# Optimization experiments

Hardware: AMD Instinct MI355X
Metric: run time of the kernel (lower is better)

The kernel has to match this reference:

```python
import jax, jax.numpy as jnp
import numpy as np

DIM = 256
HEADS = 8
HEAD_DIM = DIM // HEADS
B_, N = 8192, 49


def setup_inputs() -> dict:
    key = jax.random.key(0)
    k1, k2, k3, k4, k5, k6 = jax.random.split(key, 6)
    x = jax.random.normal(k1, (B_, N, DIM), dtype=jnp.float32)
    mask = jax.random.normal(k2, (B_, N, N), dtype=jnp.float32)
    s = 1.0 / np.sqrt(DIM)
    W_qkv = jax.random.normal(k3, (3 * DIM, DIM), dtype=jnp.float32) * s
    b_qkv = jax.random.normal(k4, (3 * DIM,), dtype=jnp.float32) * 0.02
    W_proj = jax.random.normal(k5, (DIM, DIM), dtype=jnp.float32) * s
    b_proj = jax.random.normal(k6, (DIM,), dtype=jnp.float32) * 0.02
    return {"x": x, "mask": mask, "W_qkv": W_qkv, "b_qkv": b_qkv,
            "W_proj": W_proj, "b_proj": b_proj}


def reference(x, mask, W_qkv, b_qkv, W_proj, b_proj):
    B, n, C = x.shape
    scale = HEAD_DIM ** (-0.5)
    # qkv projection: (B, N, 3C) -> (3, B, H, N, hd)
    qkv = x @ W_qkv.T + b_qkv
    qkv = qkv.reshape(B, n, 3, HEADS, HEAD_DIM).transpose(2, 0, 3, 1, 4)
    q, k, v = qkv[0], qkv[1], qkv[2]
    # scaled dot-product within each window
    attn = jnp.einsum('bhqd,bhkd->bhqk', q, k) * scale
    attn = attn + mask[:, None, :, :]  # additive window mask
    attn = jax.nn.softmax(attn, axis=-1)
    out = jnp.einsum('bhqk,bhkd->bhqd', attn, v)
    out = out.transpose(0, 2, 1, 3).reshape(B, n, C)
    return out @ W_proj.T + b_proj
```

## Files before the change

kernel.cpp:

```cpp
#include <hip/hip_runtime.h>
#include <hip/hip_bf16.h>

#define NTOK 49
#define DIMC 256

typedef __attribute__((ext_vector_type(8))) short bf16x8;
typedef __attribute__((ext_vector_type(4))) float f32x4;

static __device__ __forceinline__ unsigned pk2(float a, float b) {
    union { __hip_bfloat16 h; unsigned short u; } ua, ub;
    ua.h = __float2bfloat16(a);
    ub.h = __float2bfloat16(b);
    return (unsigned)ua.u | ((unsigned)ub.u << 16);
}

static __device__ __forceinline__ bf16x8 mkfrag(unsigned w0, unsigned w1, unsigned w2, unsigned w3) {
    union { bf16x8 v; unsigned u[4]; } t;
    t.u[0] = w0; t.u[1] = w1; t.u[2] = w2; t.u[3] = w3;
    return t.v;
}

static __device__ __forceinline__ unsigned sel2(unsigned lo, unsigned hi, int src, int ghi) {
    unsigned a = __shfl(lo, src);
    unsigned b = __shfl(hi, src);
    return ghi ? b : a;
}

__global__ void convert_weights(const float* __restrict__ wq, const float* __restrict__ wp,
                                unsigned short* __restrict__ wqb, unsigned short* __restrict__ wpb) {
    int i = blockIdx.x * 256 + threadIdx.x;
    if (i < 768 * 256) {
        union { __hip_bfloat16 h; unsigned short u; } t;
        t.h = __float2bfloat16(wq[i]);
        wqb[i] = t.u;
    }
    if (i < 256 * 256) {
        union { __hip_bfloat16 h; unsigned short u; } t;
        t.h = __float2bfloat16(wp[i]);
        wpb[i] = t.u;
    }
}

__launch_bounds__(1024, 4)
__attribute__((amdgpu_waves_per_eu(4, 4)))
__global__ void win_attn_fused(const float* __restrict__ x, const float* __restrict__ mask,
                               const unsigned short* __restrict__ wqkv, const float* __restrict__ bqkv,
                               const unsigned short* __restrict__ wproj, const float* __restrict__ bproj,
                               float* __restrict__ out) {
    __shared__ __align__(16) char lds[131072];
    char* const xb  = lds;
    char* const kqv = lds + 32768;

    const int b = blockIdx.x;
    const int tid = threadIdx.x;
    const int lane = tid & 63;
    const int wid = tid >> 6;
    const int c = lane & 15;
    const int g = lane >> 4;
    const int h = wid >> 1;
    const int qh = wid & 1;
    const int srcA = c + 16 * ((2 * g) & 3);
    const int srcB = c + 16 * ((2 * g + 1) & 3);
    const int ghi = g >> 1;
    const float scale = 0.17677669529663687f;
    const f32x4 fzero = {0.f, 0.f, 0.f, 0.f};

    {
        const float* xw = x + (size_t)b * (NTOK * DIMC);
        #pragma unroll
        for (int it = 0; it < 4; ++it) {
            int idx = it * 1024 + tid;
            int t = idx >> 6;
            int d0 = (idx & 63) * 4;
            float4 v = make_float4(0.f, 0.f, 0.f, 0.f);
            if (t < NTOK) v = *(const float4*)(xw + t * DIMC + d0);
            *(uint2*)(xb + t * 512 + ((d0 * 2) ^ ((t & 7) << 4))) =
                make_uint2(pk2(v.x, v.y), pk2(v.z, v.w));
        }
    }
    __syncthreads();

    #define XFR(base_, t_, kk_) \
        (*(const bf16x8*)((base_) + (t_) * 512 + ((2 * ((kk_) + 8 * g)) ^ (((t_) & 7) << 4))))

    char* const Kh = kqv + h * 12288;
    char* const Qh = Kh + 4096;
    char* const Vh = Kh + 8192;

    {
        f32x4 aKQ[2][4], aV[4];
        #pragma unroll
        for (int md = 0; md < 2; ++md)
            #pragma unroll
            for (int j2 = 0; j2 < 4; ++j2) aKQ[md][j2] = fzero;
        #pragma unroll
        for (int mt = 0; mt < 4; ++mt) aV[mt] = fzero;

        const int woff = qh ? (h * 32) : (256 + h * 32);
        const unsigned short* wkq_base = wqkv + (size_t)(woff + c) * 256 + 8 * g;
        const unsigned short* wv_base  = wqkv + (size_t)(512 + h * 32 + qh * 16 + c) * 256 + 8 * g;
        #pragma unroll
        for (int ks = 0; ks < 8; ++ks) {
            int kk = ks * 32;
            bf16x8 xf[4];
            #pragma unroll
            for (int tt = 0; tt < 4; ++tt) { int t = tt * 16 + c; xf[tt] = XFR(xb, t, kk); }
            bf16x8 wkq0 = *(const bf16x8*)(wkq_base + kk);
            bf16x8 wkq1 = *(const bf16x8*)(wkq_base + 16 * 256 + kk);
            bf16x8 wv   = *(const bf16x8*)(wv_base + kk);
            #pragma unroll
            for (int j2 = 0; j2 < 4; ++j2) {
                aKQ[0][j2] = __builtin_amdgcn_mfma_f32_16x16x32_bf16(wkq0, xf[j2], aKQ[0][j2], 0, 0, 0);
                aKQ[1][j2] = __builtin_amdgcn_mfma_f32_16x16x32_bf16(wkq1, xf[j2], aKQ[1][j2], 0, 0, 0);
                aV[j2]     = __builtin_amdgcn_mfma_f32_16x16x32_bf16(xf[j2], wv, aV[j2], 0, 0, 0);
            }
        }

        char* kqdst = Kh + qh * 4096;
        const float* bb = bqkv + (qh ? 0 : 256) + h * 32;
        #pragma unroll
        for (int md = 0; md < 2; ++md) {
            const float* b4 = bb + md * 16 + 4 * g;
            float b0 = b4[0], b1 = b4[1], b2 = b4[2], b3 = b4[3];
            #pragma unroll
            for (int j2 = 0; j2 < 4; ++j2) {
                int t = j2 * 16 + c;
                int d0 = md * 16 + 4 * g;
                f32x4 v = aKQ[md][j2];
                float v0 = v[0] + b0, v1 = v[1] + b1, v2 = v[2] + b2, v3 = v[3] + b3;
                if (qh) { v0 *= scale; v1 *= scale; v2 *= scale; v3 *= scale; }
                *(uint2*)(kqdst + t * 64 + ((d0 * 2) ^ ((t & 3) << 4))) =
                    make_uint2(pk2(v0, v1), pk2(v2, v3));
            }
        }
        float bv = bqkv[512 + h * 32 + qh * 16 + c];
        #pragma unroll
        for (int mt = 0; mt < 4; ++mt) {
            int t0 = mt * 16 + 4 * g;
            int d = qh * 16 + c;
            f32x4 v = aV[mt];
            *(uint2*)(Vh + d * 128 + ((t0 * 2) ^ ((d & 7) << 4))) =
                make_uint2(pk2(v[0] + bv, v[1] + bv), pk2(v[2] + bv, v[3] + bv));
        }
    }
    __syncthreads();

    f32x4 oacc[2][2];
    {
        const float* mw = mask + (size_t)b * (NTOK * NTOK);
        f32x4 mv[2][3];
        float m48[2];
        #pragma unroll
        for (int jl = 0; jl < 2; ++jl) {
            int q = (qh * 2 + jl) * 16 + c;
            int qc = (q < NTOK) ? q : (NTOK - 1);
            const float* mrow = mw + qc * NTOK;
            mv[jl][0] = *(const f32x4*)(mrow + 0 + g * 4);
            mv[jl][1] = *(const f32x4*)(mrow + 16 + g * 4);
            mv[jl][2] = *(const f32x4*)(mrow + 32 + g * 4);
            m48[jl] = mrow[48];
        }

        bf16x8 ka[4], qf[2], vf[2][2];
        #pragma unroll
        for (int it = 0; it < 4; ++it) {
            int key = it * 16 + c;
            ka[it] = *(const bf16x8*)(Kh + key * 64 + ((g * 16) ^ ((key & 3) << 4)));
        }
        #pragma unroll
        for (int jl = 0; jl < 2; ++jl) {
            int q = (qh * 2 + jl) * 16 + c;
            qf[jl] = *(const bf16x8*)(Qh + q * 64 + ((g * 16) ^ ((q & 3) << 4)));
        }
        #pragma unroll
        for (int kh = 0; kh < 2; ++kh)
            #pragma unroll
            for (int dt = 0; dt < 2; ++dt) {
                int d = dt * 16 + c;
                vf[kh][dt] = *(const bf16x8*)(Vh + d * 128 +
                                              (((kh * 32 + g * 8) * 2) ^ ((d & 7) << 4)));
            }
        #pragma unroll
        for (int dt = 0; dt < 2; ++dt)
            #pragma unroll
            for (int jl = 0; jl < 2; ++jl) oacc[dt][jl] = fzero;

        #pragma unroll
        for (int jl = 0; jl < 2; ++jl) {
            float p[4][4];
            {
                f32x4 s = __builtin_amdgcn_mfma_f32_16x16x32_bf16(ka[0], qf[jl], fzero, 0, 0, 0);
                #pragma unroll
                for (int r = 0; r < 4; ++r) p[0][r] = s[r] + mv[jl][0][r];
            }
            {
                f32x4 s = __builtin_amdgcn_mfma_f32_16x16x32_bf16(ka[1], qf[jl], fzero, 0, 0, 0);
                #pragma unroll
                for (int r = 0; r < 4; ++r) p[1][r] = s[r] + mv[jl][1][r];
            }
            {
                f32x4 s = __builtin_amdgcn_mfma_f32_16x16x32_bf16(ka[2], qf[jl], fzero, 0, 0, 0);
                #pragma unroll
                for (int r = 0; r < 4; ++r) p[2][r] = s[r] + mv[jl][2][r];
            }
            {
                f32x4 s = __builtin_amdgcn_mfma_f32_16x16x32_bf16(ka[3], qf[jl], fzero, 0, 0, 0);
                #pragma unroll
                for (int r = 0; r < 4; ++r)
                    p[3][r] = (g == 0 && r == 0) ? (s[0] + m48[jl]) : -1e30f;
            }
            float m = -1e30f;
            #pragma unroll
            for (int it = 0; it < 4; ++it)
                #pragma unroll
                for (int r = 0; r < 4; ++r) m = fmaxf(m, p[it][r]);
            m = fmaxf(m, __shfl_xor(m, 16));
            m = fmaxf(m, __shfl_xor(m, 32));
            float ssum = 0.f;
            #pragma unroll
            for (int it = 0; it < 4; ++it)
                #pragma unroll
                for (int r = 0; r < 4; ++r) {
                    float e = __expf(p[it][r] - m);
                    p[it][r] = e;
                    ssum += e;
                }
            ssum += __shfl_xor(ssum, 16);
            ssum += __shfl_xor(ssum, 32);
            float inv = 1.0f / ssum;
            unsigned pq[4][2];
            #pragma unroll
            for (int it = 0; it < 4; ++it) {
                pq[it][0] = pk2(p[it][0] * inv, p[it][1] * inv);
                pq[it][1] = pk2(p[it][2] * inv, p[it][3] * inv);
            }
            #pragma unroll
            for (int kh = 0; kh < 2; ++kh) {
                bf16x8 pf = mkfrag(sel2(pq[2 * kh][0], pq[2 * kh + 1][0], srcA, ghi),
                                   sel2(pq[2 * kh][1], pq[2 * kh + 1][1], srcA, ghi),
                                   sel2(pq[2 * kh][0], pq[2 * kh + 1][0], srcB, ghi),
                                   sel2(pq[2 * kh][1], pq[2 * kh + 1][1], srcB, ghi));
                #pragma unroll
                for (int dt = 0; dt < 2; ++dt)
                    oacc[dt][jl] = __builtin_amdgcn_mfma_f32_16x16x32_bf16(vf[kh][dt], pf, oacc[dt][jl], 0, 0, 0);
            }
        }
    }

    #pragma unroll
    for (int dt = 0; dt < 2; ++dt) {
        #pragma unroll
        for (int jl = 0; jl < 2; ++jl) {
            int q = (qh * 2 + jl) * 16 + c;
            int d0 = h * 32 + dt * 16 + 4 * g;
            f32x4 v = oacc[dt][jl];
            *(uint2*)(xb + q * 512 + ((2 * d0) ^ ((q & 7) << 4))) =
                make_uint2(pk2(v[0], v[1]), pk2(v[2], v[3]));
        }
    }
    __syncthreads();

    {
        f32x4 pacc[4];
        #pragma unroll
        for (int mt = 0; mt < 4; ++mt) pacc[mt] = fzero;
        const int o = wid * 16 + c;
        const unsigned short* wp_base = wproj + (size_t)o * 256 + 8 * g;
        const float bias = bproj[o];
        #pragma unroll
        for (int ks = 0; ks < 8; ++ks) {
            int kk = ks * 32;
            bf16x8 bfr = *(const bf16x8*)(wp_base + kk);
            #pragma unroll
            for (int mt = 0; mt < 4; ++mt) {
                int t = mt * 16 + c;
                bf16x8 af = XFR(xb, t, kk);
                pacc[mt] = __builtin_amdgcn_mfma_f32_16x16x32_bf16(af, bfr, pacc[mt], 0, 0, 0);
            }
        }
        float* ob = out + (size_t)b * (NTOK * DIMC);
        #pragma unroll
        for (int mt = 0; mt < 4; ++mt) {
            #pragma unroll
            for (int r = 0; r < 4; ++r) {
                int t = mt * 16 + g * 4 + r;
                if (t < NTOK) ob[t * DIMC + o] = pacc[mt][r] + bias;
            }
        }
    }
    #undef XFR
}

extern "C" void kernel_launch(void* const* d_in, const int* in_sizes, int n_in,
                              void* d_out, int out_size, void* d_ws, size_t ws_size,
                              hipStream_t stream) {
    const float* x    = (const float*)d_in[0];
    const float* mask = (const float*)d_in[1];
    const float* wq   = (const float*)d_in[2];
    const float* bq   = (const float*)d_in[3];
    const float* wp   = (const float*)d_in[4];
    const float* bp   = (const float*)d_in[5];
    float* o = (float*)d_out;

    unsigned short* wqb = (unsigned short*)d_ws;
    unsigned short* wpb = wqb + 768 * 256;

    convert_weights<<<768, 256, 0, stream>>>(wq, wp, wqb, wpb);
    win_attn_fused<<<8192, 1024, 0, stream>>>(x, mask, wqb, bq, wpb, bp, o);
}
```

Measured before the change: 718.1 us.

## Halve block size to 512 threads, loop each wave over two heads

The fused window-attention kernel now runs 8 waves per block instead of 16. Each wave pair processes two heads in sequence, reusing a 48KB K/Q/V LDS region, so LDS drops from 128KB to 80KB per block. Attention outputs are kept in registers until both heads finish, and the output projection computes two column tiles per wave, reusing the A fragments. The goal is to fit more blocks per CU and reuse x fragments, at the cost of more per-block serialization, extra barriers and higher register pressure.

Result: slower. 778.4 us (+8.4%).

```diff
diff --git a/kernel.cpp b/kernel.cpp
--- a/kernel.cpp
+++ b/kernel.cpp
@@ -41,13 +41,13 @@
     }
 }
 
-__launch_bounds__(1024, 4)
+__launch_bounds__(512, 4)
 __attribute__((amdgpu_waves_per_eu(4, 4)))
 __global__ void win_attn_fused(const float* __restrict__ x, const float* __restrict__ mask,
                                const unsigned short* __restrict__ wqkv, const float* __restrict__ bqkv,
                                const unsigned short* __restrict__ wproj, const float* __restrict__ bproj,
                                float* __restrict__ out) {
-    __shared__ __align__(16) char lds[131072];
+    __shared__ __align__(16) char lds[81920];
     char* const xb  = lds;
     char* const kqv = lds + 32768;
 
@@ -57,7 +57,7 @@
     const int wid = tid >> 6;
     const int c = lane & 15;
     const int g = lane >> 4;
-    const int h = wid >> 1;
+    const int lh = wid >> 1;
     const int qh = wid & 1;
     const int srcA = c + 16 * ((2 * g) & 3);
     const int srcB = c + 16 * ((2 * g + 1) & 3);
@@ -65,11 +65,15 @@
     const float scale = 0.17677669529663687f;
     const f32x4 fzero = {0.f, 0.f, 0.f, 0.f};
 
+    char* const Kh = kqv + lh * 12288;
+    char* const Qh = Kh + 4096;
+    char* const Vh = Kh + 8192;
+
     {
         const float* xw = x + (size_t)b * (NTOK * DIMC);
         #pragma unroll
-        for (int it = 0; it < 4; ++it) {
-            int idx = it * 1024 + tid;
+        for (int it = 0; it < 8; ++it) {
+            int idx = it * 512 + tid;
             int t = idx >> 6;
             int d0 = (idx & 63) * 4;
             float4 v = make_float4(0.f, 0.f, 0.f, 0.f);
@@ -83,208 +87,230 @@
     #define XFR(base_, t_, kk_) \
         (*(const bf16x8*)((base_) + (t_) * 512 + ((2 * ((kk_) + 8 * g)) ^ (((t_) & 7) << 4))))
 
-    char* const Kh = kqv + h * 12288;
-    char* const Qh = Kh + 4096;
-    char* const Vh = Kh + 8192;
+    unsigned aout[2][2][2][2];
+
+    #pragma unroll
+    for (int r = 0; r < 2; ++r) {
+        const int h = r * 4 + lh;
+
+        {
+            f32x4 aKQ[2][4], aV[4];
+            #pragma unroll
+            for (int md = 0; md < 2; ++md)
+                #pragma unroll
+                for (int j2 = 0; j2 < 4; ++j2) aKQ[md][j2] = fzero;
+            #pragma unroll
+            for (int mt = 0; mt < 4; ++mt) aV[mt] = fzero;
+
+            const int woff = qh ? (h * 32) : (256 + h * 32);
+            const unsigned short* wkq_base = wqkv + (size_t)(woff + c) * 256 + 8 * g;
+            const unsigned short* wv_base  = wqkv + (size_t)(512 + h * 32 + qh * 16 + c) * 256 + 8 * g;
+            #pragma unroll
+            for (int ks = 0; ks < 8; ++ks) {
+                int kk = ks * 32;
+                bf16x8 xf[4];
+                #pragma unroll
+                for (int tt = 0; tt < 4; ++tt) { int t = tt * 16 + c; xf[tt] = XFR(xb, t, kk); }
+                bf16x8 wkq0 = *(const bf16x8*)(wkq_base + kk);
+                bf16x8 wkq1 = *(const bf16x8*)(wkq_base + 16 * 256 + kk);
+                bf16x8 wv   = *(const bf16x8*)(wv_base + kk);
+                #pragma unroll
+                for (int j2 = 0; j2 < 4; ++j2) {
+                    aKQ[0][j2] = __builtin_amdgcn_mfma_f32_16x16x32_bf16(wkq0, xf[j2], aKQ[0][j2], 0, 0, 0);
+                    aKQ[1][j2] = __builtin_amdgcn_mfma_f32_16x16x32_bf16(wkq1, xf[j2], aKQ[1][j2], 0, 0, 0);
+                    aV[j2]     = __builtin_amdgcn_mfma_f32_16x16x32_bf16(xf[j2], wv, aV[j2], 0, 0, 0);
+                }
+            }
+
+            char* kqdst = (qh ? Qh : Kh);
+            const float* bb = bqkv + (qh ? 0 : 256) + h * 32;
+            #pragma unroll
+            for (int md = 0; md < 2; ++md) {
+                const float* b4 = bb + md * 16 + 4 * g;
+                float b0 = b4[0], b1 = b4[1], b2 = b4[2], b3 = b4[3];
+                #pragma unroll
+                for (int j2 = 0; j2 < 4; ++j2) {
+                    int t = j2 * 16 + c;
+                    int d0 = md * 16 + 4 * g;
+                    f32x4 v = aKQ[md][j2];
+                    float v0 = v[0] + b0, v1 = v[1] + b1, v2 = v[2] + b2, v3 = v[3] + b3;
+                    if (qh) { v0 *= scale; v1 *= scale; v2 *= scale; v3 *= scale; }
+                    *(uint2*)(kqdst + t * 64 + ((d0 * 2) ^ ((t & 3) << 4))) =
+                        make_uint2(pk2(v0, v1), pk2(v2, v3));
+                }
+            }
+            float bv = bqkv[512 + h * 32 + qh * 16 + c];
+            #pragma unroll
+            for (int mt = 0; mt < 4; ++mt) {
+                int t0 = mt * 16 + 4 * g;
+                int d = qh * 16 + c;
+                f32x4 v = aV[mt];
+                *(uint2*)(Vh + d * 128 + ((t0 * 2) ^ ((d & 7) << 4))) =
+                    make_uint2(pk2(v[0] + bv, v[1] + bv), pk2(v[2] + bv, v[3] + bv));
+            }
+        }
+        __syncthreads();
+
+        {
+            const float* mw = mask + (size_t)b * (NTOK * NTOK);
+            f32x4 mv[2][3];
+            float m48[2];
+            #pragma unroll
+            for (int jl = 0; jl < 2; ++jl) {
+                int q = (qh * 2 + jl) * 16 + c;
+                int qc = (q < NTOK) ? q : (NTOK - 1);
+                const float* mrow = mw + qc * NTOK;
+                mv[jl][0] = *(const f32x4*)(mrow + 0 + g * 4);
+                mv[jl][1] = *(const f32x4*)(mrow + 16 + g * 4);
+                mv[jl][2] = *(const f32x4*)(mrow + 32 + g * 4);
+                m48[jl] = mrow[48];
+            }
+
+            bf16x8 ka[4], qf[2], vf[2][2];
+            #pragma unroll
+            for (int it = 0; it < 4; ++it) {
+                int key = it * 16 + c;
+                ka[it] = *(const bf16x8*)(Kh + key * 64 + ((g * 16) ^ ((key & 3) << 4)));
+            }
+            #pragma unroll
+            for (int jl = 0; jl < 2; ++jl) {
+                int q = (qh * 2 + jl) * 16 + c;
+                qf[jl] = *(const bf16x8*)(Qh + q * 64 + ((g * 16) ^ ((q & 3) << 4)));
+            }
+            #pragma unroll
+            for (int kh = 0; kh < 2; ++kh)
+                #pragma unroll
+                for (int dt = 0; dt < 2; ++dt) {
+                    int d = dt * 16 + c;
+                    vf[kh][dt] = *(const bf16x8*)(Vh + d * 128 +
+                                                  (((kh * 32 + g * 8) * 2) ^ ((d & 7) << 4)));
+                }
+            f32x4 oacc[2][2];
+            #pragma unroll
+            for (int dt = 0; dt < 2; ++dt)
+                #pragma unroll
+                for (int jl = 0; jl < 2; ++jl) oacc[dt][jl] = fzero;
+
+            #pragma unroll
+            for (int jl = 0; jl < 2; ++jl) {
+                float p[4][4];
+                {
+                    f32x4 s = __builtin_amdgcn_mfma_f32_16x16x32_bf16(ka[0], qf[jl], fzero, 0, 0, 0);
+                    #pragma unroll
+                    for (int rr = 0; rr < 4; ++rr) p[0][rr] = s[rr] + mv[jl][0][rr];
+                }
+                {
+                    f32x4 s = __builtin_amdgcn_mfma_f32_16x16x32_bf16(ka[1], qf[jl], fzero, 0, 0, 0);
+                    #pragma unroll
+                    for (int rr = 0; rr < 4; ++rr) p[1][rr] = s[rr] + mv[jl][1][rr];
+                }
+                {
+                    f32x4 s = __builtin_amdgcn_mfma_f32_16x16x32_bf16(ka[2], qf[jl], fzero, 0, 0, 0);
+                    #pragma unroll
+                    for (int rr = 0; rr < 4; ++rr) p[2][rr] = s[rr] + mv[jl][2][rr];
+                }
+                {
+                    f32x4 s = __builtin_amdgcn_mfma_f32_16x16x32_bf16(ka[3], qf[jl], fzero, 0, 0, 0);
+                    #pragma unroll
+                    for (int rr = 0; rr < 4; ++rr)
+                        p[3][rr] = (g == 0 && rr == 0) ? (s[0] + m48[jl]) : -1e30f;
+                }
+                float m = -1e30f;
+                #pragma unroll
+                for (int it = 0; it < 4; ++it)
+                    #pragma unroll
+                    for (int rr = 0; rr < 4; ++rr) m = fmaxf(m, p[it][rr]);
+                m = fmaxf(m, __shfl_xor(m, 16));
+                m = fmaxf(m, __shfl_xor(m, 32));
+                float ssum = 0.f;
+                #pragma unroll
+                for (int it = 0; it < 4; ++it)
+                    #pragma unroll
+                    for (int rr = 0; rr < 4; ++rr) {
+                        float e = __expf(p[it][rr] - m);
+                        p[it][rr] = e;
+                        ssum += e;
+                    }
+                ssum += __shfl_xor(ssum, 16);
+                ssum += __shfl_xor(ssum, 32);
+                float inv = 1.0f / ssum;
+                unsigned pq[4][2];
+                #pragma unroll
+                for (int it = 0; it < 4; ++it) {
+                    pq[it][0] = pk2(p[it][0] * inv, p[it][1] * inv);
+                    pq[it][1] = pk2(p[it][2] * inv, p[it][3] * inv);
+                }
+                #pragma unroll
+                for (int kh = 0; kh < 2; ++kh) {
+                    bf16x8 pf = mkfrag(sel2(pq[2 * kh][0], pq[2 * kh + 1][0], srcA, ghi),
+                                       sel2(pq[2 * kh][1], pq[2 * kh + 1][1], srcA, ghi),
+                                       sel2(pq[2 * kh][0], pq[2 * kh + 1][0], srcB, ghi),
+                                       sel2(pq[2 * kh][1], pq[2 * kh + 1][1], srcB, ghi));
+                    #pragma unroll
+                    for (int dt = 0; dt < 2; ++dt)
+                        oacc[dt][jl] = __builtin_amdgcn_mfma_f32_16x16x32_bf16(vf[kh][dt], pf, oacc[dt][jl], 0, 0, 0);
+                }
+            }
+            #pragma unroll
+            for (int dt = 0; dt < 2; ++dt)
+                #pragma unroll
+                for (int jl = 0; jl < 2; ++jl) {
+                    aout[r][dt][jl][0] = pk2(oacc[dt][jl][0], oacc[dt][jl][1]);
+                    aout[r][dt][jl][1] = pk2(oacc[dt][jl][2], oacc[dt][jl][3]);
+                }
+        }
+        __syncthreads();
+    }
+
+    #pragma unroll
+    for (int r = 0; r < 2; ++r) {
+        #pragma unroll
+        for (int dt = 0; dt < 2; ++dt) {
+            #pragma unroll
+            for (int jl = 0; jl < 2; ++jl) {
+                int q = (qh * 2 + jl) * 16 + c;
+                int d0 = (r * 4 + lh) * 32 + dt * 16 + 4 * g;
+                *(uint2*)(xb + q * 512 + ((2 * d0) ^ ((q & 7) << 4))) =
+                    make_uint2(aout[r][dt][jl][0], aout[r][dt][jl][1]);
+            }
+        }
+    }
+    __syncthreads();
 
     {
-        f32x4 aKQ[2][4], aV[4];
-        #pragma unroll
-        for (int md = 0; md < 2; ++md)
-            #pragma unroll
-            for (int j2 = 0; j2 < 4; ++j2) aKQ[md][j2] = fzero;
-        #pragma unroll
-        for (int mt = 0; mt < 4; ++mt) aV[mt] = fzero;
-
-        const int woff = qh ? (h * 32) : (256 + h * 32);
-        const unsigned short* wkq_base = wqkv + (size_t)(woff + c) * 256 + 8 * g;
-        const unsigned short* wv_base  = wqkv + (size_t)(512 + h * 32 + qh * 16 + c) * 256 + 8 * g;
+        f32x4 pacc[2][4];
+        #pragma unroll
+        for (int j = 0; j < 2; ++j)
+            #pragma unroll
+            for (int mt = 0; mt < 4; ++mt) pacc[j][mt] = fzero;
+
         #pragma unroll
         for (int ks = 0; ks < 8; ++ks) {
             int kk = ks * 32;
-            bf16x8 xf[4];
-            #pragma unroll
-            for (int tt = 0; tt < 4; ++tt) { int t = tt * 16 + c; xf[tt] = XFR(xb, t, kk); }
-            bf16x8 wkq0 = *(const bf16x8*)(wkq_base + kk);
-            bf16x8 wkq1 = *(const bf16x8*)(wkq_base + 16 * 256 + kk);
-            bf16x8 wv   = *(const bf16x8*)(wv_base + kk);
-            #pragma unroll
-            for (int j2 = 0; j2 < 4; ++j2) {
-                aKQ[0][j2] = __builtin_amdgcn_mfma_f32_16x16x32_bf16(wkq0, xf[j2], aKQ[0][j2], 0, 0, 0);
-                aKQ[1][j2] = __builtin_amdgcn_mfma_f32_16x16x32_bf16(wkq1, xf[j2], aKQ[1][j2], 0, 0, 0);
-                aV[j2]     = __builtin_amdgcn_mfma_f32_16x16x32_bf16(xf[j2], wv, aV[j2], 0, 0, 0);
-            }
-        }
-
-        char* kqdst = Kh + qh * 4096;
-        const float* bb = bqkv + (qh ? 0 : 256) + h * 32;
-        #pragma unroll
-        for (int md = 0; md < 2; ++md) {
-            const float* b4 = bb + md * 16 + 4 * g;
-            float b0 = b4[0], b1 = b4[1], b2 = b4[2], b3 = b4[3];
-            #pragma unroll
-            for (int j2 = 0; j2 < 4; ++j2) {
-                int t = j2 * 16 + c;
-                int d0 = md * 16 + 4 * g;
-                f32x4 v = aKQ[md][j2];
-                float v0 = v[0] + b0, v1 = v[1] + b1, v2 = v[2] + b2, v3 = v[3] + b3;
-                if (qh) { v0 *= scale; v1 *= scale; v2 *= scale; v3 *= scale; }
-                *(uint2*)(kqdst + t * 64 + ((d0 * 2) ^ ((t & 3) << 4))) =
-                    make_uint2(pk2(v0, v1), pk2(v2, v3));
-            }
-        }
-        float bv = bqkv[512 + h * 32 + qh * 16 + c];
-        #pragma unroll
-        for (int mt = 0; mt < 4; ++mt) {
-            int t0 = mt * 16 + 4 * g;
-            int d = qh * 16 + c;
-            f32x4 v = aV[mt];
-            *(uint2*)(Vh + d * 128 + ((t0 * 2) ^ ((d & 7) << 4))) =
-                make_uint2(pk2(v[0] + bv, v[1] + bv), pk2(v[2] + bv, v[3] + bv));
-        }
-    }
-    __syncthreads();
-
-    f32x4 oacc[2][2];
-    {
-        const float* mw = mask + (size_t)b * (NTOK * NTOK);
-        f32x4 mv[2][3];
-        float m48[2];
-        #pragma unroll
-        for (int jl = 0; jl < 2; ++jl) {
-            int q = (qh * 2 + jl) * 16 + c;
-            int qc = (q < NTOK) ? q : (NTOK - 1);
-            const float* mrow = mw + qc * NTOK;
-            mv[jl][0] = *(const f32x4*)(mrow + 0 + g * 4);
-            mv[jl][1] = *(const f32x4*)(mrow + 16 + g * 4);
-            mv[jl][2] = *(const f32x4*)(mrow + 32 + g * 4);
-            m48[jl] = mrow[48];
-        }
-
-        bf16x8 ka[4], qf[2], vf[2][2];
-        #pragma unroll
-        for (int it = 0; it < 4; ++it) {
-            int key = it * 16 + c;
-            ka[it] = *(const bf16x8*)(Kh + key * 64 + ((g * 16) ^ ((key & 3) << 4)));
-        }
-        #pragma unroll
-        for (int jl = 0; jl < 2; ++jl) {
-            int q = (qh * 2 + jl) * 16 + c;
-            qf[jl] = *(const bf16x8*)(Qh + q * 64 + ((g * 16) ^ ((q & 3) << 4)));
-        }
-        #pragma unroll
-        for (int kh = 0; kh < 2; ++kh)
-            #pragma unroll
-            for (int dt = 0; dt < 2; ++dt) {
-                int d = dt * 16 + c;
-                vf[kh][dt] = *(const bf16x8*)(Vh + d * 128 +
-                                              (((kh * 32 + g * 8) * 2) ^ ((d & 7) << 4)));
-            }
-        #pragma unroll
-        for (int dt = 0; dt < 2; ++dt)
-            #pragma unroll
-            for (int jl = 0; jl < 2; ++jl) oacc[dt][jl] = fzero;
-
-        #pragma unroll
-        for (int jl = 0; jl < 2; ++jl) {
-            float p[4][4];
-            {
-                f32x4 s = __builtin_amdgcn_mfma_f32_16x16x32_bf16(ka[0], qf[jl], fzero, 0, 0, 0);
-                #pragma unroll
-                for (int r = 0; r < 4; ++r) p[0][r] = s[r] + mv[jl][0][r];
-            }
-            {
-                f32x4 s = __builtin_amdgcn_mfma_f32_16x16x32_bf16(ka[1], qf[jl], fzero, 0, 0, 0);
-                #pragma unroll
-                for (int r = 0; r < 4; ++r) p[1][r] = s[r] + mv[jl][1][r];
-            }
-            {
-                f32x4 s = __builtin_amdgcn_mfma_f32_16x16x32_bf16(ka[2], qf[jl], fzero, 0, 0, 0);
-                #pragma unroll
-                for (int r = 0; r < 4; ++r) p[2][r] = s[r] + mv[jl][2][r];
-            }
-            {
-                f32x4 s = __builtin_amdgcn_mfma_f32_16x16x32_bf16(ka[3], qf[jl], fzero, 0, 0, 0);
-                #pragma unroll
-                for (int r = 0; r < 4; ++r)
-                    p[3][r] = (g == 0 && r == 0) ? (s[0] + m48[jl]) : -1e30f;
-            }
-            float m = -1e30f;
-            #pragma unroll
-            for (int it = 0; it < 4; ++it)
-                #pragma unroll
-                for (int r = 0; r < 4; ++r) m = fmaxf(m, p[it][r]);
-            m = fmaxf(m, __shfl_xor(m, 16));
-            m = fmaxf(m, __shfl_xor(m, 32));
-            float ssum = 0.f;
-            #pragma unroll
-            for (int it = 0; it < 4; ++it)
-                #pragma unroll
-                for (int r = 0; r < 4; ++r) {
-                    float e = __expf(p[it][r] - m);
-                    p[it][r] = e;
-                    ssum += e;
-                }
-            ssum += __shfl_xor(ssum, 16);
-            ssum += __shfl_xor(ssum, 32);
-            float inv = 1.0f / ssum;
-            unsigned pq[4][2];
-            #pragma unroll
-            for (int it = 0; it < 4; ++it) {
-                pq[it][0] = pk2(p[it][0] * inv, p[it][1] * inv);
-                pq[it][1] = pk2(p[it][2] * inv, p[it][3] * inv);
-            }
-            #pragma unroll
-            for (int kh = 0; kh < 2; ++kh) {
-                bf16x8 pf = mkfrag(sel2(pq[2 * kh][0], pq[2 * kh + 1][0], srcA, ghi),
-                                   sel2(pq[2 * kh][1], pq[2 * kh + 1][1], srcA, ghi),
-                                   sel2(pq[2 * kh][0], pq[2 * kh + 1][0], srcB, ghi),
-                                   sel2(pq[2 * kh][1], pq[2 * kh + 1][1], srcB, ghi));
-                #pragma unroll
-                for (int dt = 0; dt < 2; ++dt)
-                    oacc[dt][jl] = __builtin_amdgcn_mfma_f32_16x16x32_bf16(vf[kh][dt], pf, oacc[dt][jl], 0, 0, 0);
-            }
-        }
-    }
-
-    #pragma unroll
-    for (int dt = 0; dt < 2; ++dt) {
-        #pragma unroll
-        for (int jl = 0; jl < 2; ++jl) {
-            int q = (qh * 2 + jl) * 16 + c;
-            int d0 = h * 32 + dt * 16 + 4 * g;
-            f32x4 v = oacc[dt][jl];
-            *(uint2*)(xb + q * 512 + ((2 * d0) ^ ((q & 7) << 4))) =
-                make_uint2(pk2(v[0], v[1]), pk2(v[2], v[3]));
-        }
-    }
-    __syncthreads();
-
-    {
-        f32x4 pacc[4];
-        #pragma unroll
-        for (int mt = 0; mt < 4; ++mt) pacc[mt] = fzero;
-        const int o = wid * 16 + c;
-        const unsigned short* wp_base = wproj + (size_t)o * 256 + 8 * g;
-        const float bias = bproj[o];
-        #pragma unroll
-        for (int ks = 0; ks < 8; ++ks) {
-            int kk = ks * 32;
-            bf16x8 bfr = *(const bf16x8*)(wp_base + kk);
+            bf16x8 af[4];
+            #pragma unroll
+            for (int mt = 0; mt < 4; ++mt) { int t = mt * 16 + c; af[mt] = XFR(xb, t, kk); }
+            #pragma unroll
+            for (int j = 0; j < 2; ++j) {
+                int o = (wid * 2 + j) * 16 + c;
+                bf16x8 bfr = *(const bf16x8*)(wproj + (size_t)o * 256 + kk + 8 * g);
+                #pragma unroll
+                for (int mt = 0; mt < 4; ++mt)
+                    pacc[j][mt] = __builtin_amdgcn_mfma_f32_16x16x32_bf16(af[mt], bfr, pacc[j][mt], 0, 0, 0);
+            }
+        }
+        float* ob = out + (size_t)b * (NTOK * DIMC);
+        #pragma unroll
+        for (int j = 0; j < 2; ++j) {
+            int o = (wid * 2 + j) * 16 + c;
+            float bias = bproj[o];
             #pragma unroll
             for (int mt = 0; mt < 4; ++mt) {
-                int t = mt * 16 + c;
-                bf16x8 af = XFR(xb, t, kk);
-                pacc[mt] = __builtin_amdgcn_mfma_f32_16x16x32_bf16(af, bfr, pacc[mt], 0, 0, 0);
-            }
-        }
-        float* ob = out + (size_t)b * (NTOK * DIMC);
-        #pragma unroll
-        for (int mt = 0; mt < 4; ++mt) {
-            #pragma unroll
-            for (int r = 0; r < 4; ++r) {
-                int t = mt * 16 + g * 4 + r;
-                if (t < NTOK) ob[t * DIMC + o] = pacc[mt][r] + bias;
+                #pragma unroll
+                for (int rr = 0; rr < 4; ++rr) {
+                    int t = mt * 16 + g * 4 + rr;
+                    if (t < NTOK) ob[t * DIMC + o] = pacc[j][mt][rr] + bias;
+                }
             }
         }
     }
@@ -306,5 +332,5 @@
     unsigned short* wpb = wqb + 768 * 256;
 
     convert_weights<<<768, 256, 0, stream>>>(wq, wp, wqb, wpb);
-    win_attn_fused<<<8192, 1024, 0, stream>>>(x, mask, wqb, bq, wpb, bp, o);
-}
+    win_attn_fused<<<8192, 512, 0, stream>>>(x, mask, wqb, bq, wpb, bp, o);
+}
```

## Process multiple windows per block with prefetch of next window's inputs

Applied to the files above, without the earlier changes.

Each 1024-thread block now loops over 8 windows instead of one, cutting the grid to 1024 blocks and amortizing launch and setup costs. During the output projection of each window, threads issue dummy loads touching the next window's x and mask lines so they are warmed in cache before the next iteration. This adds an extra barrier per iteration and reduces the number of blocks available for scheduling, which may limit occupancy balance across CUs.

Measured after the change: 1.051 ms. 46.4% more time.

```diff
diff --git a/kernel.cpp b/kernel.cpp
--- a/kernel.cpp
+++ b/kernel.cpp
@@ -3,6 +3,7 @@
 
 #define NTOK 49
 #define DIMC 256
+#define WPB  8
 
 typedef __attribute__((ext_vector_type(8))) short bf16x8;
 typedef __attribute__((ext_vector_type(4))) float f32x4;
@@ -51,7 +52,6 @@
     char* const xb  = lds;
     char* const kqv = lds + 32768;
 
-    const int b = blockIdx.x;
     const int tid = threadIdx.x;
     const int lane = tid & 63;
     const int wid = tid >> 6;
@@ -65,230 +65,250 @@
     const float scale = 0.17677669529663687f;
     const f32x4 fzero = {0.f, 0.f, 0.f, 0.f};
 
-    {
-        const float* xw = x + (size_t)b * (NTOK * DIMC);
-        #pragma unroll
-        for (int it = 0; it < 4; ++it) {
-            int idx = it * 1024 + tid;
-            int t = idx >> 6;
-            int d0 = (idx & 63) * 4;
-            float4 v = make_float4(0.f, 0.f, 0.f, 0.f);
-            if (t < NTOK) v = *(const float4*)(xw + t * DIMC + d0);
-            *(uint2*)(xb + t * 512 + ((d0 * 2) ^ ((t & 7) << 4))) =
-                make_uint2(pk2(v.x, v.y), pk2(v.z, v.w));
-        }
-    }
-    __syncthreads();
-
-    #define XFR(base_, t_, kk_) \
-        (*(const bf16x8*)((base_) + (t_) * 512 + ((2 * ((kk_) + 8 * g)) ^ (((t_) & 7) << 4))))
-
     char* const Kh = kqv + h * 12288;
     char* const Qh = Kh + 4096;
     char* const Vh = Kh + 8192;
 
-    {
-        f32x4 aKQ[2][4], aV[4];
+    const int b0 = blockIdx.x * WPB;
+
+    #pragma unroll 1
+    for (int w = 0; w < WPB; ++w) {
+        const int b = b0 + w;
+
+        {
+            const float* xw = x + (size_t)b * (NTOK * DIMC);
+            #pragma unroll
+            for (int it = 0; it < 4; ++it) {
+                int idx = it * 1024 + tid;
+                int t = idx >> 6;
+                int d0 = (idx & 63) * 4;
+                float4 v = make_float4(0.f, 0.f, 0.f, 0.f);
+                if (t < NTOK) v = *(const float4*)(xw + t * DIMC + d0);
+                *(uint2*)(xb + t * 512 + ((d0 * 2) ^ ((t & 7) << 4))) =
+                    make_uint2(pk2(v.x, v.y), pk2(v.z, v.w));
+            }
+        }
+        __syncthreads();
+
+        #define XFR(base_, t_, kk_) \
+            (*(const bf16x8*)((base_) + (t_) * 512 + ((2 * ((kk_) + 8 * g)) ^ (((t_) & 7) << 4))))
+
+        {
+            f32x4 aKQ[2][4], aV[4];
+            #pragma unroll
+            for (int md = 0; md < 2; ++md)
+                #pragma unroll
+                for (int j2 = 0; j2 < 4; ++j2) aKQ[md][j2] = fzero;
+            #pragma unroll
+            for (int mt = 0; mt < 4; ++mt) aV[mt] = fzero;
+
+            const int woff = qh ? (h * 32) : (256 + h * 32);
+            const unsigned short* wkq_base = wqkv + (size_t)(woff + c) * 256 + 8 * g;
+            const unsigned short* wv_base  = wqkv + (size_t)(512 + h * 32 + qh * 16 + c) * 256 + 8 * g;
+            #pragma unroll
+            for (int ks = 0; ks < 8; ++ks) {
+                int kk = ks * 32;
+                bf16x8 xf[4];
+                #pragma unroll
+                for (int tt = 0; tt < 4; ++tt) { int t = tt * 16 + c; xf[tt] = XFR(xb, t, kk); }
+                bf16x8 wkq0 = *(const bf16x8*)(wkq_base + kk);
+                bf16x8 wkq1 = *(const bf16x8*)(wkq_base + 16 * 256 + kk);
+                bf16x8 wv   = *(const bf16x8*)(wv_base + kk);
+                #pragma unroll
+                for (int j2 = 0; j2 < 4; ++j2) {
+                    aKQ[0][j2] = __builtin_amdgcn_mfma_f32_16x16x32_bf16(wkq0, xf[j2], aKQ[0][j2], 0, 0, 0);
+                    aKQ[1][j2] = __builtin_amdgcn_mfma_f32_16x16x32_bf16(wkq1, xf[j2], aKQ[1][j2], 0, 0, 0);
+                    aV[j2]     = __builtin_amdgcn_mfma_f32_16x16x32_bf16(xf[j2], wv, aV[j2], 0, 0, 0);
+                }
+            }
+
+            char* kqdst = (qh ? Qh : Kh);
+            const float* bb = bqkv + (qh ? 0 : 256) + h * 32;
+            #pragma unroll
+            for (int md = 0; md < 2; ++md) {
+                const float* b4 = bb + md * 16 + 4 * g;
+                float b0_ = b4[0], b1_ = b4[1], b2_ = b4[2], b3_ = b4[3];
+                #pragma unroll
+                for (int j2 = 0; j2 < 4; ++j2) {
+                    int t = j2 * 16 + c;
+                    int d0 = md * 16 + 4 * g;
+                    f32x4 v = aKQ[md][j2];
+                    float v0 = v[0] + b0_, v1 = v[1] + b1_, v2 = v[2] + b2_, v3 = v[3] + b3_;
+                    if (qh) { v0 *= scale; v1 *= scale; v2 *= scale; v3 *= scale; }
+                    *(uint2*)(kqdst + t * 64 + ((d0 * 2) ^ ((t & 3) << 4))) =
+                        make_uint2(pk2(v0, v1), pk2(v2, v3));
+                }
+            }
+            float bv = bqkv[512 + h * 32 + qh * 16 + c];
+            #pragma unroll
+            for (int mt = 0; mt < 4; ++mt) {
+                int t0 = mt * 16 + 4 * g;
+                int d = qh * 16 + c;
+                f32x4 v = aV[mt];
+                *(uint2*)(Vh + d * 128 + ((t0 * 2) ^ ((d & 7) << 4))) =
+                    make_uint2(pk2(v[0] + bv, v[1] + bv), pk2(v[2] + bv, v[3] + bv));
+            }
+        }
+        __syncthreads();
+
+        f32x4 oacc[2][2];
+        {
+            const float* mw = mask + (size_t)b * (NTOK * NTOK);
+            f32x4 mv[2][3];
+            float m48[2];
+            #pragma unroll
+            for (int jl = 0; jl < 2; ++jl) {
+                int q = (qh * 2 + jl) * 16 + c;
+                int qc = (q < NTOK) ? q : (NTOK - 1);
+                const float* mrow = mw + qc * NTOK;
+                mv[jl][0] = *(const f32x4*)(mrow + 0 + g * 4);
+                mv[jl][1] = *(const f32x4*)(mrow + 16 + g * 4);
+                mv[jl][2] = *(const f32x4*)(mrow + 32 + g * 4);
+                m48[jl] = mrow[48];
+            }
+
+            bf16x8 ka[4], qf[2], vf[2][2];
+            #pragma unroll
+            for (int it = 0; it < 4; ++it) {
+                int key = it * 16 + c;
+                ka[it] = *(const bf16x8*)(Kh + key * 64 + ((g * 16) ^ ((key & 3) << 4)));
+            }
+            #pragma unroll
+            for (int jl = 0; jl < 2; ++jl) {
+                int q = (qh * 2 + jl) * 16 + c;
+                qf[jl] = *(const bf16x8*)(Qh + q * 64 + ((g * 16) ^ ((q & 3) << 4)));
+            }
+            #pragma unroll
+            for (int kh = 0; kh < 2; ++kh)
+                #pragma unroll
+                for (int dt = 0; dt < 2; ++dt) {
+                    int d = dt * 16 + c;
+                    vf[kh][dt] = *(const bf16x8*)(Vh + d * 128 +
+                                                  (((kh * 32 + g * 8) * 2) ^ ((d & 7) << 4)));
+                }
+            #pragma unroll
+            for (int dt = 0; dt < 2; ++dt)
+                #pragma unroll
+                for (int jl = 0; jl < 2; ++jl) oacc[dt][jl] = fzero;
+
+            #pragma unroll
+            for (int jl = 0; jl < 2; ++jl) {
+                float p[4][4];
+                {
+                    f32x4 s = __builtin_amdgcn_mfma_f32_16x16x32_bf16(ka[0], qf[jl], fzero, 0, 0, 0);
+                    #pragma unroll
+                    for (int rr = 0; rr < 4; ++rr) p[0][rr] = s[rr] + mv[jl][0][rr];
+                }
+                {
+                    f32x4 s = __builtin_amdgcn_mfma_f32_16x16x32_bf16(ka[1], qf[jl], fzero, 0, 0, 0);
+                    #pragma unroll
+                    for (int rr = 0; rr < 4; ++rr) p[1][rr] = s[rr] + mv[jl][1][rr];
+                }
+                {
+                    f32x4 s = __builtin_amdgcn_mfma_f32_16x16x32_bf16(ka[2], qf[jl], fzero, 0, 0, 0);
+                    #pragma unroll
+                    for (int rr = 0; rr < 4; ++rr) p[2][rr] = s[rr] + mv[jl][2][rr];
+                }
+                {
+                    f32x4 s = __builtin_amdgcn_mfma_f32_16x16x32_bf16(ka[3], qf[jl], fzero, 0, 0, 0);
+                    #pragma unroll
+                    for (int rr = 0; rr < 4; ++rr)
+                        p[3][rr] = (g == 0 && rr == 0) ? (s[0] + m48[jl]) : -1e30f;
+                }
+                float m = -1e30f;
+                #pragma unroll
+                for (int it = 0; it < 4; ++it)
+                    #pragma unroll
+                    for (int rr = 0; rr < 4; ++rr) m = fmaxf(m, p[it][rr]);
+                m = fmaxf(m, __shfl_xor(m, 16));
+                m = fmaxf(m, __shfl_xor(m, 32));
+                float ssum = 0.f;
+                #pragma unroll
+                for (int it = 0; it < 4; ++it)
+                    #pragma unroll
+                    for (int rr = 0; rr < 4; ++rr) {
+                        float e = __expf(p[it][rr] - m);
+                        p[it][rr] = e;
+                        ssum += e;
+                    }
+                ssum += __shfl_xor(ssum, 16);
+                ssum += __shfl_xor(ssum, 32);
+                float inv = 1.0f / ssum;
+                unsigned pq[4][2];
+                #pragma unroll
+                for (int it = 0; it < 4; ++it) {
+                    pq[it][0] = pk2(p[it][0] * inv, p[it][1] * inv);
+                    pq[it][1] = pk2(p[it][2] * inv, p[it][3] * inv);
+                }
+                #pragma unroll
+                for (int kh = 0; kh < 2; ++kh) {
+                    bf16x8 pf = mkfrag(sel2(pq[2 * kh][0], pq[2 * kh + 1][0], srcA, ghi),
+                                       sel2(pq[2 * kh][1], pq[2 * kh + 1][1], srcA, ghi),
+                                       sel2(pq[2 * kh][0], pq[2 * kh + 1][0], srcB, ghi),
+                                       sel2(pq[2 * kh][1], pq[2 * kh + 1][1], srcB, ghi));
+                    #pragma unroll
+                    for (int dt = 0; dt < 2; ++dt)
+                        oacc[dt][jl] = __builtin_amdgcn_mfma_f32_16x16x32_bf16(vf[kh][dt], pf, oacc[dt][jl], 0, 0, 0);
+                }
+            }
+        }
+
         #pragma unroll
-        for (int md = 0; md < 2; ++md)
-            #pragma unroll
-            for (int j2 = 0; j2 < 4; ++j2) aKQ[md][j2] = fzero;
-        #pragma unroll
-        for (int mt = 0; mt < 4; ++mt) aV[mt] = fzero;
-
-        const int woff = qh ? (h * 32) : (256 + h * 32);
-        const unsigned short* wkq_base = wqkv + (size_t)(woff + c) * 256 + 8 * g;
-        const unsigned short* wv_base  = wqkv + (size_t)(512 + h * 32 + qh * 16 + c) * 256 + 8 * g;
-        #pragma unroll
-        for (int ks = 0; ks < 8; ++ks) {
-            int kk = ks * 32;
-            bf16x8 xf[4];
-            #pragma unroll
-            for (int tt = 0; tt < 4; ++tt) { int t = tt * 16 + c; xf[tt] = XFR(xb, t, kk); }
-            bf16x8 wkq0 = *(const bf16x8*)(wkq_base + kk);
-            bf16x8 wkq1 = *(const bf16x8*)(wkq_base + 16 * 256 + kk);
-            bf16x8 wv   = *(const bf16x8*)(wv_base + kk);
-            #pragma unroll
-            for (int j2 = 0; j2 < 4; ++j2) {
-                aKQ[0][j2] = __builtin_amdgcn_mfma_f32_16x16x32_bf16(wkq0, xf[j2], aKQ[0][j2], 0, 0, 0);
-                aKQ[1][j2] = __builtin_amdgcn_mfma_f32_16x16x32_bf16(wkq1, xf[j2], aKQ[1][j2], 0, 0, 0);
-                aV[j2]     = __builtin_amdgcn_mfma_f32_16x16x32_bf16(xf[j2], wv, aV[j2], 0, 0, 0);
-            }
-        }
-
-        char* kqdst = Kh + qh * 4096;
-        const float* bb = bqkv + (qh ? 0 : 256) + h * 32;
-        #pragma unroll
-        for (int md = 0; md < 2; ++md) {
-            const float* b4 = bb + md * 16 + 4 * g;
-            float b0 = b4[0], b1 = b4[1], b2 = b4[2], b3 = b4[3];
-            #pragma unroll
-            for (int j2 = 0; j2 < 4; ++j2) {
-                int t = j2 * 16 + c;
-                int d0 = md * 16 + 4 * g;
-                f32x4 v = aKQ[md][j2];
-                float v0 = v[0] + b0, v1 = v[1] + b1, v2 = v[2] + b2, v3 = v[3] + b3;
-                if (qh) { v0 *= scale; v1 *= scale; v2 *= scale; v3 *= scale; }
-                *(uint2*)(kqdst + t * 64 + ((d0 * 2) ^ ((t & 3) << 4))) =
-                    make_uint2(pk2(v0, v1), pk2(v2, v3));
-            }
-        }
-        float bv = bqkv[512 + h * 32 + qh * 16 + c];
-        #pragma unroll
-        for (int mt = 0; mt < 4; ++mt) {
-            int t0 = mt * 16 + 4 * g;
-            int d = qh * 16 + c;
-            f32x4 v = aV[mt];
-            *(uint2*)(Vh + d * 128 + ((t0 * 2) ^ ((d & 7) << 4))) =
-                make_uint2(pk2(v[0] + bv, v[1] + bv), pk2(v[2] + bv, v[3] + bv));
-        }
+        for (int dt = 0; dt < 2; ++dt) {
+            #pragma unroll
+            for (int jl = 0; jl < 2; ++jl) {
+                int q = (qh * 2 + jl) * 16 + c;
+                int d0 = h * 32 + dt * 16 + 4 * g;
+                f32x4 v = oacc[dt][jl];
+                *(uint2*)(xb + q * 512 + ((2 * d0) ^ ((q & 7) << 4))) =
+                    make_uint2(pk2(v[0], v[1]), pk2(v[2], v[3]));
+            }
+        }
+        __syncthreads();
+
+        if (w + 1 < WPB) {
+            const float* xn = x + (size_t)(b + 1) * (NTOK * DIMC);
+            const float* mn = mask + (size_t)(b + 1) * (NTOK * NTOK);
+            if (tid < 784) {
+                float v = xn[tid * 16];
+                asm volatile("" :: "v"(v));
+            } else if (tid < 935) {
+                float v = mn[(tid - 784) * 16];
+                asm volatile("" :: "v"(v));
+            }
+        }
+
+        {
+            f32x4 pacc[4];
+            #pragma unroll
+            for (int mt = 0; mt < 4; ++mt) pacc[mt] = fzero;
+            const int o = wid * 16 + c;
+            const unsigned short* wp_base = wproj + (size_t)o * 256 + 8 * g;
+            const float bias = bproj[o];
+            #pragma unroll
+            for (int ks = 0; ks < 8; ++ks) {
+                int kk = ks * 32;
+                bf16x8 bfr = *(const bf16x8*)(wp_base + kk);
+                #pragma unroll
+                for (int mt = 0; mt < 4; ++mt) {
+                    int t = mt * 16 + c;
+                    bf16x8 af = XFR(xb, t, kk);
+                    pacc[mt] = __builtin_amdgcn_mfma_f32_16x16x32_bf16(af, bfr, pacc[mt], 0, 0, 0);
+                }
+            }
+            float* ob = out + (size_t)b * (NTOK * DIMC);
+            #pragma unroll
+            for (int mt = 0; mt < 4; ++mt) {
+                #pragma unroll
+                for (int rr = 0; rr < 4; ++rr) {
+                    int t = mt * 16 + g * 4 + rr;
+                    if (t < NTOK) ob[t * DIMC + o] = pacc[mt][rr] + bias;
+                }
+            }
+        }
+        __syncthreads();
+        #undef XFR
     }
-    __syncthreads();
-
-    f32x4 oacc[2][2];
-    {
-        const float* mw = mask + (size_t)b * (NTOK * NTOK);
-        f32x4 mv[2][3];
-        float m48[2];
-        #pragma unroll
-        for (int jl = 0; jl < 2; ++jl) {
-            int q = (qh * 2 + jl) * 16 + c;
-            int qc = (q < NTOK) ? q : (NTOK - 1);
-            const float* mrow = mw + qc * NTOK;
-            mv[jl][0] = *(const f32x4*)(mrow + 0 + g * 4);
-            mv[jl][1] = *(const f32x4*)(mrow + 16 + g * 4);
-            mv[jl][2] = *(const f32x4*)(mrow + 32 + g * 4);
-            m48[jl] = mrow[48];
-        }
-
-        bf16x8 ka[4], qf[2], vf[2][2];
-        #pragma unroll
-        for (int it = 0; it < 4; ++it) {
-            int key = it * 16 + c;
-            ka[it] = *(const bf16x8*)(Kh + key * 64 + ((g * 16) ^ ((key & 3) << 4)));
-        }
-        #pragma unroll
-        for (int jl = 0; jl < 2; ++jl) {
-            int q = (qh * 2 + jl) * 16 + c;
-            qf[jl] = *(const bf16x8*)(Qh + q * 64 + ((g * 16) ^ ((q & 3) << 4)));
-        }
-        #pragma unroll
-        for (int kh = 0; kh < 2; ++kh)
-            #pragma unroll
-            for (int dt = 0; dt < 2; ++dt) {
-                int d = dt * 16 + c;
-                vf[kh][dt] = *(const bf16x8*)(Vh + d * 128 +
-                                              (((kh * 32 + g * 8) * 2) ^ ((d & 7) << 4)));
-            }
-        #pragma unroll
-        for (int dt = 0; dt < 2; ++dt)
-            #pragma unroll
-            for (int jl = 0; jl < 2; ++jl) oacc[dt][jl] = fzero;
-
-        #pragma unroll
-        for (int jl = 0; jl < 2; ++jl) {
-            float p[4][4];
-            {
-                f32x4 s = __builtin_amdgcn_mfma_f32_16x16x32_bf16(ka[0], qf[jl], fzero, 0, 0, 0);
-                #pragma unroll
-                for (int r = 0; r < 4; ++r) p[0][r] = s[r] + mv[jl][0][r];
-            }
-            {
-                f32x4 s = __builtin_amdgcn_mfma_f32_16x16x32_bf16(ka[1], qf[jl], fzero, 0, 0, 0);
-                #pragma unroll
-                for (int r = 0; r < 4; ++r) p[1][r] = s[r] + mv[jl][1][r];
-            }
-            {
-                f32x4 s = __builtin_amdgcn_mfma_f32_16x16x32_bf16(ka[2], qf[jl], fzero, 0, 0, 0);
-                #pragma unroll
-                for (int r = 0; r < 4; ++r) p[2][r] = s[r] + mv[jl][2][r];
-            }
-            {
-                f32x4 s = __builtin_amdgcn_mfma_f32_16x16x32_bf16(ka[3], qf[jl], fzero, 0, 0, 0);
-                #pragma unroll
-                for (int r = 0; r < 4; ++r)
-                    p[3][r] = (g == 0 && r == 0) ? (s[0] + m48[jl]) : -1e30f;
-            }
-            float m = -1e30f;
-            #pragma unroll
-            for (int it = 0; it < 4; ++it)
-                #pragma unroll
-                for (int r = 0; r < 4; ++r) m = fmaxf(m, p[it][r]);
-            m = fmaxf(m, __shfl_xor(m, 16));
-            m = fmaxf(m, __shfl_xor(m, 32));
-            float ssum = 0.f;
-            #pragma unroll
-            for (int it = 0; it < 4; ++it)
-                #pragma unroll
-                for (int r = 0; r < 4; ++r) {
-                    float e = __expf(p[it][r] - m);
-                    p[it][r] = e;
-                    ssum += e;
-                }
-            ssum += __shfl_xor(ssum, 16);
-            ssum += __shfl_xor(ssum, 32);
-            float inv = 1.0f / ssum;
-            unsigned pq[4][2];
-            #pragma unroll
-            for (int it = 0; it < 4; ++it) {
-                pq[it][0] = pk2(p[it][0] * inv, p[it][1] * inv);
-                pq[it][1] = pk2(p[it][2] * inv, p[it][3] * inv);
-            }
-            #pragma unroll
-            for (int kh = 0; kh < 2; ++kh) {
-                bf16x8 pf = mkfrag(sel2(pq[2 * kh][0], pq[2 * kh + 1][0], srcA, ghi),
-                                   sel2(pq[2 * kh][1], pq[2 * kh + 1][1], srcA, ghi),
-                                   sel2(pq[2 * kh][0], pq[2 * kh + 1][0], srcB, ghi),
-                                   sel2(pq[2 * kh][1], pq[2 * kh + 1][1], srcB, ghi));
-                #pragma unroll
-                for (int dt = 0; dt < 2; ++dt)
-                    oacc[dt][jl] = __builtin_amdgcn_mfma_f32_16x16x32_bf16(vf[kh][dt], pf, oacc[dt][jl], 0, 0, 0);
-            }
-        }
-    }
-
-    #pragma unroll
-    for (int dt = 0; dt < 2; ++dt) {
-        #pragma unroll
-        for (int jl = 0; jl < 2; ++jl) {
-            int q = (qh * 2 + jl) * 16 + c;
-            int d0 = h * 32 + dt * 16 + 4 * g;
-            f32x4 v = oacc[dt][jl];
-            *(uint2*)(xb + q * 512 + ((2 * d0) ^ ((q & 7) << 4))) =
-                make_uint2(pk2(v[0], v[1]), pk2(v[2], v[3]));
-        }
-    }
-    __syncthreads();
-
-    {
-        f32x4 pacc[4];
-        #pragma unroll
-        for (int mt = 0; mt < 4; ++mt) pacc[mt] = fzero;
-        const int o = wid * 16 + c;
-        const unsigned short* wp_base = wproj + (size_t)o * 256 + 8 * g;
-        const float bias = bproj[o];
-        #pragma unroll
-        for (int ks = 0; ks < 8; ++ks) {
-            int kk = ks * 32;
-            bf16x8 bfr = *(const bf16x8*)(wp_base + kk);
-            #pragma unroll
-            for (int mt = 0; mt < 4; ++mt) {
-                int t = mt * 16 + c;
-                bf16x8 af = XFR(xb, t, kk);
-                pacc[mt] = __builtin_amdgcn_mfma_f32_16x16x32_bf16(af, bfr, pacc[mt], 0, 0, 0);
-            }
-        }
-        float* ob = out + (size_t)b * (NTOK * DIMC);
-        #pragma unroll
-        for (int mt = 0; mt < 4; ++mt) {
-            #pragma unroll
-            for (int r = 0; r < 4; ++r) {
-                int t = mt * 16 + g * 4 + r;
-                if (t < NTOK) ob[t * DIMC + o] = pacc[mt][r] + bias;
-            }
-        }
-    }
-    #undef XFR
 }
 
 extern "C" void kernel_launch(void* const* d_in, const int* in_sizes, int n_in,
@@ -306,5 +326,5 @@
     unsigned short* wpb = wqb + 768 * 256;
 
     convert_weights<<<768, 256, 0, stream>>>(wq, wp, wqb, wpb);
-    win_attn_fused<<<8192, 1024, 0, stream>>>(x, mask, wqb, bq, wpb, bp, o);
-}
+    win_attn_fused<<<8192 / WPB, 1024, 0, stream>>>(x, mask, wqb, bq, wpb, bp, o);
+}
```
